# Optimization experiments

Measured on AMD Instinct MI355X. Metric: run time of the kernel, lower is better.

The kernel has to match this reference:

```python
import jax, jax.numpy as jnp
import numpy as np

B, T, D, H, L, V, CTX = 4, 2048, 256, 8, 12, 256, 2048
HD = D // H


def _ln(x, w, b, eps=1e-5):
    m = x.mean(-1, keepdims=True)
    v = ((x - m) ** 2).mean(-1, keepdims=True)
    return (x - m) * jax.lax.rsqrt(v + eps) * w + b


def setup_inputs() -> dict:
    key = jax.random.key(0)
    ks = jax.random.split(key, 16)
    s = 0.02
    inp = {
        "x": jax.random.randint(ks[0], (B, T), 0, V, dtype=jnp.int32),
        "tok_embed": jax.random.normal(ks[1], (V, D), jnp.float32) * s,
        "pos_embed": jax.random.normal(ks[2], (CTX, D), jnp.float32) * s,
        # stacked per-layer params (leading axis = layer)
        "ln1_w": jnp.ones((L, D), jnp.float32),
        "ln1_b": jnp.zeros((L, D), jnp.float32),
        "qkv_w": jax.random.normal(ks[3], (L, D, 3 * D), jnp.float32) * s,
        "qkv_b": jnp.zeros((L, 3 * D), jnp.float32),
        "out_w": jax.random.normal(ks[4], (L, D, D), jnp.float32) * s,
        "out_b": jnp.zeros((L, D), jnp.float32),
        "ln2_w": jnp.ones((L, D), jnp.float32),
        "ln2_b": jnp.zeros((L, D), jnp.float32),
        "fc1_w": jax.random.normal(ks[5], (L, D, 4 * D), jnp.float32) * s,
        "fc1_b": jnp.zeros((L, 4 * D), jnp.float32),
        "fc2_w": jax.random.normal(ks[6], (L, 4 * D, D), jnp.float32) * s,
        "fc2_b": jnp.zeros((L, D), jnp.float32),
        "lnf_w": jnp.ones((D,), jnp.float32),
        "lnf_b": jnp.zeros((D,), jnp.float32),
        "head_w": jax.random.normal(ks[7], (D, V), jnp.float32) * s,
        "head_b": jnp.zeros((V,), jnp.float32),
    }
    return inp


def _forward(x, tok_embed, pos_embed, ln1_w, ln1_b, qkv_w, qkv_b, out_w, out_b,
             ln2_w, ln2_b, fc1_w, fc1_b, fc2_w, fc2_b, lnf_w, lnf_b, head_w, head_b):
    Tcur = x.shape[1]
    h = tok_embed[x] + pos_embed[:Tcur][None, :, :]  # (B,T,D)
    causal = jnp.triu(jnp.ones((Tcur, Tcur), bool), k=1)  # True above diagonal
    scale = jnp.sqrt(jnp.asarray(HD, h.dtype))

    def step(h, p):
        (l1w, l1b, qw, qb, ow, ob, l2w, l2b, f1w, f1b, f2w, f2b) = p
        # attention
        z = _ln(h, l1w, l1b)
        qkv = z @ qw + qb  # (B,T,3D)
        qkv = qkv.reshape(h.shape[0], Tcur, 3, H, HD)
        q, k, v = qkv[:, :, 0], qkv[:, :, 1], qkv[:, :, 2]  # (B,T,H,HD)
        attn = jnp.einsum('bqhd,bkhd->bhqk', q, k) / scale
        attn = jnp.where(causal, -jnp.inf, attn)
        attn = jax.nn.softmax(attn, axis=-1)
        o = jnp.einsum('bhqk,bkhd->bqhd', attn, v).reshape(h.shape[0], Tcur, D)
        h = h + o @ ow + ob
        # MLP (torch nn.GELU default = exact erf gelu)
        z = _ln(h, l2w, l2b)
        z = jax.nn.gelu(z @ f1w + f1b, approximate=False)
        h = h + z @ f2w + f2b
        return h, None

    params = (ln1_w, ln1_b, qkv_w, qkv_b, out_w, out_b,
              ln2_w, ln2_b, fc1_w, fc1_b, fc2_w, fc2_b)
    h, _ = jax.lax.scan(step, h, params)
    h = _ln(h, lnf_w, lnf_b)
    return h @ head_w + head_b  # (B,T,V)


def reference(x, tok_embed, pos_embed, ln1_w, ln1_b, qkv_w, qkv_b, out_w, out_b,
              ln2_w, ln2_b, fc1_w, fc1_b, fc2_w, fc2_b, lnf_w, lnf_b, head_w, head_b):
    return _forward(x, tok_embed, pos_embed, ln1_w, ln1_b, qkv_w, qkv_b, out_w, out_b,
                    ln2_w, ln2_b, fc1_w, fc1_b, fc2_w, fc2_b, lnf_w, lnf_b, head_w, head_b)
```

## Files before the change

kernel.cpp:

```cpp
#include <hip/hip_runtime.h>
#include <cstdint>

#define TT 2048
#define DD 256
#define HH 8
#define LL 12

typedef __attribute__((ext_vector_type(8))) short s16x8;
typedef __attribute__((ext_vector_type(4))) float f32x4;

__device__ __forceinline__ unsigned short f2bf(float f) {
  union { float f; unsigned u; } v; v.f = f;
  return (unsigned short)((v.u + 0x7FFFu + ((v.u >> 16) & 1u)) >> 16);
}

__device__ __forceinline__ unsigned cvtpk(float lo, float hi) {
  unsigned r;
  asm("v_cvt_pk_bf16_f32 %0, %1, %2" : "=v"(r) : "v"(lo), "v"(hi));
  return r;
}

__device__ __forceinline__ float geluf(float x) {
  return 0.5f * x * (1.0f + erff(x * 0.70710678118654752f));
}

__device__ __forceinline__ float fexp2(float x) {
  float r;
  asm("v_exp_f32 %0, %1" : "=v"(r) : "v"(x));
  return r;
}

__device__ __forceinline__ void gload16(const void* g, void* l) {
  __builtin_amdgcn_global_load_lds((const __attribute__((address_space(1))) unsigned int*)g,
                                   (__attribute__((address_space(3))) unsigned int*)l, 16, 0, 0);
}

__global__ __launch_bounds__(256) void k_embed_ln(const int* __restrict__ x,
                                                  const float* __restrict__ tok,
                                                  const float* __restrict__ pos,
                                                  const float* __restrict__ wgt,
                                                  const float* __restrict__ bia,
                                                  float* __restrict__ h,
                                                  unsigned short* __restrict__ z) {
  int row = blockIdx.x * 4 + (threadIdx.x >> 6);
  int lane = threadIdx.x & 63;
  int t = x[row];
  f32x4 tv = ((const f32x4*)(tok + (size_t)t * DD))[lane];
  f32x4 pv = ((const f32x4*)(pos + (size_t)(row & (TT - 1)) * DD))[lane];
  f32x4 v = tv + pv;
  ((f32x4*)(h + (size_t)row * DD))[lane] = v;
  float s = v[0] + v[1] + v[2] + v[3];
#pragma unroll
  for (int m = 32; m; m >>= 1) s += __shfl_xor(s, m);
  float mean = s * (1.0f / DD);
  f32x4 d = v - mean;
  float s2 = d[0] * d[0] + d[1] * d[1] + d[2] * d[2] + d[3] * d[3];
#pragma unroll
  for (int m = 32; m; m >>= 1) s2 += __shfl_xor(s2, m);
  float inv = rsqrtf(s2 * (1.0f / DD) + 1e-5f);
  f32x4 wv = ((const f32x4*)wgt)[lane];
  f32x4 bv = ((const f32x4*)bia)[lane];
  float o0 = d[0] * inv * wv[0] + bv[0], o1 = d[1] * inv * wv[1] + bv[1];
  float o2 = d[2] * inv * wv[2] + bv[2], o3 = d[3] * inv * wv[3] + bv[3];
  unsigned long long u64 = (unsigned long long)cvtpk(o0, o1) |
                           ((unsigned long long)cvtpk(o2, o3) << 32);
  *(unsigned long long*)(z + (size_t)row * DD + lane * 4) = u64;
}

__global__ __launch_bounds__(256) void k_cast_all(const float* __restrict__ qw, const float* __restrict__ ow,
                                                  const float* __restrict__ f1, const float* __restrict__ f2,
                                                  const float* __restrict__ hw,
                                                  unsigned short* __restrict__ dst) {
  __shared__ float Tt[32][33];
  const int l = blockIdx.y;
  const int t = blockIdx.x;
  const float* src;
  unsigned short* d;
  int K, N, tk, tn;
  if (l == 12) {
    if (t >= 64) return;
    src = hw; d = dst + (size_t)12 * 786432;
    K = 256; N = 256; tk = t >> 3; tn = t & 7;
  } else if (t < 192) {
    src = qw + (size_t)l * 196608; d = dst + (size_t)l * 786432;
    K = 256; N = 768; tk = t / 24; tn = t % 24;
  } else if (t < 256) {
    int t2 = t - 192;
    src = ow + (size_t)l * 65536; d = dst + (size_t)l * 786432 + 196608;
    K = 256; N = 256; tk = t2 >> 3; tn = t2 & 7;
  } else if (t < 512) {
    int t3 = t - 256;
    src = f1 + (size_t)l * 262144; d = dst + (size_t)l * 786432 + 262144;
    K = 256; N = 1024; tk = t3 >> 5; tn = t3 & 31;
  } else {
    int t4 = t - 512;
    src = f2 + (size_t)l * 262144; d = dst + (size_t)l * 786432 + 524288;
    K = 1024; N = 256; tk = t4 >> 3; tn = t4 & 7;
  }
  const int tx = threadIdx.x & 31, ty = threadIdx.x >> 5;
#pragma unroll
  for (int r = 0; r < 4; ++r) {
    int row = ty + r * 8;
    Tt[row][tx] = src[(size_t)(tk * 32 + row) * N + tn * 32 + tx];
  }
  __syncthreads();
#pragma unroll
  for (int r = 0; r < 4; ++r) {
    int row = ty + r * 8;
    d[(size_t)(tn * 32 + row) * K + tk * 32 + tx] = f2bf(Tt[tx][row]);
  }
}

__global__ __launch_bounds__(256) void k_cast_tr4(const float* __restrict__ qw, const float* __restrict__ ow,
                                                  const float* __restrict__ f1, const float* __restrict__ f2,
                                                  unsigned short* __restrict__ dq, unsigned short* __restrict__ dO,
                                                  unsigned short* __restrict__ d1, unsigned short* __restrict__ d2) {
  int t0 = blockIdx.x * 256 + threadIdx.x;
  int stride = gridDim.x * 256;
  for (int i = t0; i < 196608; i += stride) dq[i] = f2bf(qw[(i & 255) * 768 + (i >> 8)]);
  for (int i = t0; i < 65536; i += stride) dO[i] = f2bf(ow[(i & 255) * 256 + (i >> 8)]);
  for (int i = t0; i < 262144; i += stride) d1[i] = f2bf(f1[(i & 255) * 1024 + (i >> 8)]);
  for (int i = t0; i < 262144; i += stride) d2[i] = f2bf(f2[(i & 1023) * 256 + (i >> 10)]);
}

__global__ __launch_bounds__(256) void k_cast_tr256(const float* __restrict__ src, unsigned short* __restrict__ dst) {
  int i = blockIdx.x * 256 + threadIdx.x;
  dst[i] = f2bf(src[(i & 255) * 256 + (i >> 8)]);
}

template <int MODE, int MI>
__global__ __launch_bounds__(256, 3) void k_gemm(const unsigned short* __restrict__ A,
                                                 const unsigned short* __restrict__ BT,
                                                 const float* __restrict__ bias,
                                                 void* out, const float* resid,
                                                 int M, int N, int K) {
  __shared__ __align__(16) unsigned short As[2][MI * 32 * 64];
  __shared__ __align__(16) unsigned short Bs[2][128 * 64];
  const int tid = threadIdx.x;
  const int lane = tid & 63, wv = tid >> 6;
  const int wr = wv >> 1, wc = wv & 1;
  const int l15 = lane & 15, g = lane >> 4;
  const int BM = MI * 32;
  const int tm = blockIdx.y, tn = blockIdx.x;
  f32x4 acc[MI][4] = {};
  const int nk = K >> 6;
  const unsigned short* Ag0 = A + (size_t)tm * BM * K;
  const unsigned short* Bg0 = BT + (size_t)tn * 128 * K;

#pragma unroll
  for (int it = 0; it < MI; ++it) {
    int c = it * 256 + tid;
    gload16(Ag0 + (size_t)(c >> 3) * K + (c & 7) * 8, As[0] + c * 8);
  }
#pragma unroll
  for (int it = 0; it < 4; ++it) {
    int c = it * 256 + tid;
    gload16(Bg0 + (size_t)(c >> 3) * K + (c & 7) * 8, Bs[0] + c * 8);
  }
  __syncthreads();

  int buf = 0;
  for (int kt = 0; kt < nk; ++kt) {
    const bool have_next = (kt + 1 < nk);
    if (have_next) {
#pragma unroll
      for (int it = 0; it < MI; ++it) {
        int c = it * 256 + tid;
        gload16(Ag0 + (size_t)(c >> 3) * K + (kt + 1) * 64 + (c & 7) * 8, As[buf ^ 1] + c * 8);
      }
#pragma unroll
      for (int it = 0; it < 4; ++it) {
        int c = it * 256 + tid;
        gload16(Bg0 + (size_t)(c >> 3) * K + (kt + 1) * 64 + (c & 7) * 8, Bs[buf ^ 1] + c * 8);
      }
    }
#pragma unroll
    for (int ks = 0; ks < 2; ++ks) {
      s16x8 af[MI], bf[4];
#pragma unroll
      for (int mi = 0; mi < MI; ++mi)
        af[mi] = *(const s16x8*)(As[buf] + (wr * MI * 16 + mi * 16 + l15) * 64 + ks * 32 + g * 8);
#pragma unroll
      for (int ni = 0; ni < 4; ++ni)
        bf[ni] = *(const s16x8*)(Bs[buf] + (wc * 64 + ni * 16 + l15) * 64 + ks * 32 + g * 8);
#pragma unroll
      for (int mi = 0; mi < MI; ++mi)
#pragma unroll
        for (int ni = 0; ni < 4; ++ni)
          acc[mi][ni] = __builtin_amdgcn_mfma_f32_16x16x32_bf16(af[mi], bf[ni], acc[mi][ni], 0, 0, 0);
    }
    if (have_next) {
      __syncthreads();
      buf ^= 1;
    }
  }
#pragma unroll
  for (int ni = 0; ni < 4; ++ni) {
    int col = tn * 128 + wc * 64 + ni * 16 + l15;
    float bv = bias[col];
#pragma unroll
    for (int mi = 0; mi < MI; ++mi) {
      int row0 = tm * BM + wr * MI * 16 + mi * 16 + g * 4;
#pragma unroll
      for (int r = 0; r < 4; ++r) {
        size_t idx = (size_t)(row0 + r) * N + col;
        float vvv = acc[mi][ni][r] + bv;
        if (MODE == 0) ((unsigned short*)out)[idx] = f2bf(vvv);
        else if (MODE == 1) ((unsigned short*)out)[idx] = f2bf(geluf(vvv));
        else ((float*)out)[idx] = vvv;
      }
    }
  }
}

template <int NK>
__global__ __launch_bounds__(512, 2) void k_gemm_ln(const unsigned short* __restrict__ A,
                                                    const unsigned short* __restrict__ BT,
                                                    const float* __restrict__ bias,
                                                    float* __restrict__ h,
                                                    const float* __restrict__ lnw,
                                                    const float* __restrict__ lnb,
                                                    unsigned short* __restrict__ z) {
  __shared__ __align__(16) unsigned short As[2][32 * 64];
  __shared__ __align__(16) unsigned short Bs[2][256 * 64];
  const int tid = threadIdx.x;
  const int lane = tid & 63, wc = tid >> 6;
  const int l15 = lane & 15, g = lane >> 4;
  const int tm = blockIdx.x;
  const int K = NK * 64;
  const int row0 = tm * 32;
  f32x4 acc[2][2] = {};
  const unsigned short* Ag0 = A + (size_t)tm * 32 * K;

  float rv[2][2][4];
#pragma unroll
  for (int mi = 0; mi < 2; ++mi)
#pragma unroll
    for (int ni = 0; ni < 2; ++ni) {
      int col = wc * 32 + ni * 16 + l15;
#pragma unroll
      for (int r = 0; r < 4; ++r)
        rv[mi][ni][r] = h[(size_t)(row0 + mi * 16 + g * 4 + r) * DD + col];
    }

  if (tid < 256) gload16(Ag0 + (size_t)(tid >> 3) * K + (tid & 7) * 8, As[0] + tid * 8);
#pragma unroll
  for (int it = 0; it < 4; ++it) {
    int c = it * 512 + tid;
    gload16(BT + (size_t)(c >> 3) * K + (c & 7) * 8, Bs[0] + c * 8);
  }
  __syncthreads();

  int buf = 0;
  for (int kt = 0; kt < NK; ++kt) {
    const bool have_next = (kt + 1 < NK);
    if (have_next) {
      if (tid < 256)
        gload16(Ag0 + (size_t)(tid >> 3) * K + (kt + 1) * 64 + (tid & 7) * 8, As[buf ^ 1] + tid * 8);
#pragma unroll
      for (int it = 0; it < 4; ++it) {
        int c = it * 512 + tid;
        gload16(BT + (size_t)(c >> 3) * K + (kt + 1) * 64 + (c & 7) * 8, Bs[buf ^ 1] + c * 8);
      }
    }
#pragma unroll
    for (int ks = 0; ks < 2; ++ks) {
      s16x8 af[2], bf[2];
#pragma unroll
      for (int mi = 0; mi < 2; ++mi)
        af[mi] = *(const s16x8*)(As[buf] + (mi * 16 + l15) * 64 + ks * 32 + g * 8);
#pragma unroll
      for (int ni = 0; ni < 2; ++ni)
        bf[ni] = *(const s16x8*)(Bs[buf] + (wc * 32 + ni * 16 + l15) * 64 + ks * 32 + g * 8);
#pragma unroll
      for (int mi = 0; mi < 2; ++mi)
#pragma unroll
        for (int ni = 0; ni < 2; ++ni)
          acc[mi][ni] = __builtin_amdgcn_mfma_f32_16x16x32_bf16(af[mi], bf[ni], acc[mi][ni], 0, 0, 0);
    }
    if (have_next) {
      __syncthreads();
      buf ^= 1;
    }
  }
  float hv[2][2][4];
  float psum[2][4] = {}, psq[2][4] = {};
#pragma unroll
  for (int mi = 0; mi < 2; ++mi)
#pragma unroll
    for (int ni = 0; ni < 2; ++ni) {
      int col = wc * 32 + ni * 16 + l15;
      float bv = bias[col];
#pragma unroll
      for (int r = 0; r < 4; ++r) {
        int row = row0 + mi * 16 + g * 4 + r;
        float v = acc[mi][ni][r] + bv + rv[mi][ni][r];
        hv[mi][ni][r] = v;
        h[(size_t)row * DD + col] = v;
        psum[mi][r] += v;
        psq[mi][r] += v * v;
      }
    }
#pragma unroll
  for (int m = 1; m < 16; m <<= 1)
#pragma unroll
    for (int mi = 0; mi < 2; ++mi)
#pragma unroll
      for (int r = 0; r < 4; ++r) {
        psum[mi][r] += __shfl_xor(psum[mi][r], m);
        psq[mi][r] += __shfl_xor(psq[mi][r], m);
      }
  __syncthreads();
  float* red = (float*)&As[0][0];
  if (l15 == 0) {
#pragma unroll
    for (int mi = 0; mi < 2; ++mi)
#pragma unroll
      for (int r = 0; r < 4; ++r) {
        int rw = mi * 16 + g * 4 + r;
        red[wc * 32 + rw] = psum[mi][r];
        red[256 + wc * 32 + rw] = psq[mi][r];
      }
  }
  __syncthreads();
  float mean[2][4], inv[2][4];
#pragma unroll
  for (int mi = 0; mi < 2; ++mi)
#pragma unroll
    for (int r = 0; r < 4; ++r) {
      int rw = mi * 16 + g * 4 + r;
      float s = 0.f, q = 0.f;
#pragma unroll
      for (int wv = 0; wv < 8; ++wv) {
        s += red[wv * 32 + rw];
        q += red[256 + wv * 32 + rw];
      }
      float mn = s * (1.0f / DD);
      mean[mi][r] = mn;
      inv[mi][r] = rsqrtf(q * (1.0f / DD) - mn * mn + 1e-5f);
    }
#pragma unroll
  for (int ni = 0; ni < 2; ++ni) {
    int col = wc * 32 + ni * 16 + l15;
    float wvv = lnw[col], bvv = lnb[col];
#pragma unroll
    for (int mi = 0; mi < 2; ++mi)
#pragma unroll
      for (int r = 0; r < 4; ++r) {
        int row = row0 + mi * 16 + g * 4 + r;
        z[(size_t)row * DD + col] = f2bf((hv[mi][ni][r] - mean[mi][r]) * inv[mi][r] * wvv + bvv);
      }
  }
}

__global__ __launch_bounds__(512, 4) void k_attn(const unsigned short* __restrict__ qkv,
                                                 unsigned short* __restrict__ o) {
  __shared__ __align__(16) unsigned short Ks[2][128 * 40];
  __shared__ __align__(16) unsigned short Vs[2][2 * 32 * 72];
  const int tid = threadIdx.x, lane = tid & 63, wvi = tid >> 6;
  const int w = wvi >> 1, kh = wvi & 1;
  const int l15 = lane & 15, g = lane >> 4;
  const int p = blockIdx.x;
  const int b = blockIdx.y >> 3, hh = blockIdx.y & 7;
  const size_t base = (size_t)b * TT * 768 + hh * 32;
  const float scl2 = 0.25503492f;
  const int qt0 = p, qt1 = 31 - p;
  const int nt0 = (qt0 >> 1) + 1;
  const int krow = (wvi & 3) * 32 + (lane >> 1);
  const int khK = lane & 1;
  const int iv = wvi & 3;
  const int khv = iv >> 1, dh = iv & 1;

  s16x8 qf0 = *(const s16x8*)(qkv + base + (size_t)(qt0 * 64 + w * 16 + l15) * 768 + g * 8);
  s16x8 qf1 = *(const s16x8*)(qkv + base + (size_t)(qt1 * 64 + w * 16 + l15) * 768 + g * 8);

  if (wvi < 4) {
    const unsigned short* kp = qkv + base + (size_t)krow * 768 + 256 + khK * 16;
    s16x8 k0 = *(const s16x8*)kp;
    s16x8 k1 = *(const s16x8*)(kp + 8);
    *(s16x8*)(Ks[0] + krow * 40 + khK * 16) = k0;
    *(s16x8*)(Ks[0] + krow * 40 + khK * 16 + 8) = k1;
  } else {
    const unsigned short* vp = qkv + base + (size_t)(khv * 64 + lane) * 768 + 512 + dh * 16;
    s16x8 v0 = *(const s16x8*)vp;
    s16x8 v1 = *(const s16x8*)(vp + 8);
    unsigned short* vb = Vs[0] + khv * 2304;
#pragma unroll
    for (int e = 0; e < 8; ++e) {
      int d0 = dh * 16 + e, d1 = dh * 16 + 8 + e;
      vb[d0 * 72 + (lane ^ (((d0 >> 3) & 3) << 4))] = (unsigned short)v0[e];
      vb[d1 * 72 + (lane ^ (((d1 >> 3) & 3) << 4))] = (unsigned short)v1[e];
    }
  }
  __syncthreads();

  f32x4 accO[2] = {};
  float mM = -3.0e38f, ls = 0.f;

  for (int t = 0; t < 17; ++t) {
    const int buf = t & 1;
    const bool ph = (t >= nt0);
    const int qt = ph ? qt1 : qt0;
    const int j = ph ? t - nt0 : t;
    const bool have_next = (t + 1 < 17);
    unsigned short* ps = (wvi < 4) ? (Ks[buf ^ 1] + wvi * 1280)
                                   : (Vs[buf ^ 1] + (wvi - 4) * 1152);
    s16x8 k0n, k1n, v0n, v1n;
    if (have_next) {
      const int jn = (t + 1 >= nt0) ? t + 1 - nt0 : t + 1;
      if (wvi < 4) {
        const unsigned short* kp = qkv + base + (size_t)(jn * 128 + krow) * 768 + 256 + khK * 16;
        k0n = *(const s16x8*)kp;
        k1n = *(const s16x8*)(kp + 8);
      } else {
        const unsigned short* vp = qkv + base + (size_t)(jn * 128 + khv * 64 + lane) * 768 + 512 + dh * 16;
        v0n = *(const s16x8*)vp;
        v1n = *(const s16x8*)(vp + 8);
      }
    }
    const int rel = qt * 64 + w * 16 - j * 128;
    int cbg = (rel + 15) >> 4; if (cbg > 7) cbg = 7;
    const int cbm = (cbg - kh * 4 > 3) ? 3 : cbg - kh * 4;
    if (cbm >= 0) {
      const bool fullw = (rel >= kh * 64 + 63);
      f32x4 st[4];
#pragma unroll
      for (int c = 0; c < 4; ++c)
        if (c <= cbm) {
          s16x8 kf = *(const s16x8*)(Ks[buf] + (kh * 64 + c * 16 + l15) * 40 + g * 8);
          f32x4 zz = {};
          st[c] = __builtin_amdgcn_mfma_f32_16x16x32_bf16(kf, ph ? qf1 : qf0, zz, 0, 0, 0);
        }
      float rmax = -3.0e38f;
#pragma unroll
      for (int c = 0; c < 4; ++c)
        if (c <= cbm) {
          if (!fullw) {
#pragma unroll
            for (int r = 0; r < 4; ++r)
              if ((kh * 64 + c * 16 + g * 4 + r) > rel + l15) st[c][r] = -3.0e38f;
          }
#pragma unroll
          for (int r = 0; r < 4; ++r) rmax = fmaxf(rmax, st[c][r]);
        }
      rmax = fmaxf(rmax, __shfl_xor(rmax, 16));
      rmax = fmaxf(rmax, __shfl_xor(rmax, 32));
      const float rs = rmax * scl2;
      float al = 1.0f;
      if (!__all(rs <= mM + 11.5f)) {
        float nm = fmaxf(mM, rs);
        al = fexp2(mM - nm);
        mM = nm;
#pragma unroll
        for (int r = 0; r < 4; ++r) {
          float aw = __shfl(al, g * 4 + r);
          accO[0][r] *= aw;
          accO[1][r] *= aw;
        }
      }
      float rsum = 0.f;
#pragma unroll
      for (int c = 0; c < 4; ++c)
        if (c <= cbm) {
          float e0 = fexp2(fmaf(st[c][0], scl2, -mM));
          float e1 = fexp2(fmaf(st[c][1], scl2, -mM));
          float e2 = fexp2(fmaf(st[c][2], scl2, -mM));
          float e3 = fexp2(fmaf(st[c][3], scl2, -mM));
          rsum += (e0 + e1) + (e2 + e3);
          unsigned long long u = (unsigned long long)cvtpk(e0, e1) |
                                 ((unsigned long long)cvtpk(e2, e3) << 32);
          *(unsigned long long*)(ps + l15 * 72 + c * 16 + g * 4) = u;
        }
      if (cbm < 3 && !(cbm & 1))
        *(unsigned long long*)(ps + l15 * 72 + (cbm + 1) * 16 + g * 4) = 0ULL;
      rsum += __shfl_xor(rsum, 16);
      rsum += __shfl_xor(rsum, 32);
      ls = ls * al + rsum;
      asm volatile("s_waitcnt lgkmcnt(0)" ::: "memory");
      __builtin_amdgcn_sched_barrier(0);
      const int kcm = cbm >> 1;
#pragma unroll
      for (int kc = 0; kc < 2; ++kc)
        if (kc <= kcm) {
          s16x8 pa = *(const s16x8*)(ps + l15 * 72 + kc * 32 + g * 8);
          s16x8 bv0, bv1;
#pragma unroll
          for (int hb = 0; hb < 2; ++hb) {
            const int d = hb * 16 + l15;
            const int kx = (kc * 32 + g * 8) ^ (((d >> 3) & 3) << 4);
            if (hb == 0) bv0 = *(const s16x8*)(Vs[buf] + kh * 2304 + d * 72 + kx);
            else bv1 = *(const s16x8*)(Vs[buf] + kh * 2304 + d * 72 + kx);
          }
          accO[0] = __builtin_amdgcn_mfma_f32_16x16x32_bf16(pa, bv0, accO[0], 0, 0, 0);
          accO[1] = __builtin_amdgcn_mfma_f32_16x16x32_bf16(pa, bv1, accO[1], 0, 0, 0);
        }
    }
    if (have_next) {
      if (wvi < 4) {
        *(s16x8*)(Ks[buf ^ 1] + krow * 40 + khK * 16) = k0n;
        *(s16x8*)(Ks[buf ^ 1] + krow * 40 + khK * 16 + 8) = k1n;
      } else {
        unsigned short* vb = Vs[buf ^ 1] + khv * 2304;
#pragma unroll
        for (int e = 0; e < 8; ++e) {
          int d0 = dh * 16 + e, d1 = dh * 16 + 8 + e;
          vb[d0 * 72 + (lane ^ (((d0 >> 3) & 3) << 4))] = (unsigned short)v0n[e];
          vb[d1 * 72 + (lane ^ (((d1 >> 3) & 3) << 4))] = (unsigned short)v1n[e];
        }
      }
      __syncthreads();
    }
    if (t == nt0 - 1) {
      float* sc = (float*)((wvi < 4) ? (Ks[buf] + wvi * 1280) : (Vs[buf] + (wvi - 4) * 1152));
#pragma unroll
      for (int hb = 0; hb < 2; ++hb)
#pragma unroll
        for (int r = 0; r < 4; ++r) sc[(g * 4 + r) * 32 + hb * 16 + l15] = accO[hb][r];
      if (g == 0) { sc[512 + l15] = mM; sc[528 + l15] = ls; }
      __syncthreads();
      if (kh == 0) {
        const int pw = wvi + 1;
        float* pb = (float*)((pw < 4) ? (Ks[buf] + pw * 1280) : (Vs[buf] + (pw - 4) * 1152));
#pragma unroll
        for (int r = 0; r < 4; ++r) {
          int q = g * 4 + r;
          float mA = __shfl(mM, q), lA = __shfl(ls, q);
          float mB = pb[512 + q], lB = pb[528 + q];
          float M = fmaxf(mA, mB);
          float eA = fexp2(mA - M), eB = fexp2(mB - M);
          float inv = 1.0f / (eA * lA + eB * lB);
          int row = qt0 * 64 + w * 16 + q;
#pragma unroll
          for (int hb = 0; hb < 2; ++hb) {
            float ob = pb[q * 32 + hb * 16 + l15];
            float val = (eA * accO[hb][r] + eB * ob) * inv;
            o[(size_t)(b * TT + row) * DD + hh * 32 + hb * 16 + l15] = f2bf(val);
          }
        }
      }
      __syncthreads();
      accO[0] = f32x4{};
      accO[1] = f32x4{};
      mM = -3.0e38f;
      ls = 0.f;
    }
  }
  {
    __syncthreads();
    float* sc = (float*)((wvi < 4) ? (Ks[0] + wvi * 1280) : (Vs[0] + (wvi - 4) * 1152));
#pragma unroll
    for (int hb = 0; hb < 2; ++hb)
#pragma unroll
      for (int r = 0; r < 4; ++r) sc[(g * 4 + r) * 32 + hb * 16 + l15] = accO[hb][r];
    if (g == 0) { sc[512 + l15] = mM; sc[528 + l15] = ls; }
    __syncthreads();
    if (kh == 0) {
      const int pw = wvi + 1;
      float* pb = (float*)((pw < 4) ? (Ks[0] + pw * 1280) : (Vs[0] + (pw - 4) * 1152));
#pragma unroll
      for (int r = 0; r < 4; ++r) {
        int q = g * 4 + r;
        float mA = __shfl(mM, q), lA = __shfl(ls, q);
        float mB = pb[512 + q], lB = pb[528 + q];
        float M = fmaxf(mA, mB);
        float eA = fexp2(mA - M), eB = fexp2(mB - M);
        float inv = 1.0f / (eA * lA + eB * lB);
        int row = qt1 * 64 + w * 16 + q;
#pragma unroll
        for (int hb = 0; hb < 2; ++hb) {
          float ob = pb[q * 32 + hb * 16 + l15];
          float val = (eA * accO[hb][r] + eB * ob) * inv;
          o[(size_t)(b * TT + row) * DD + hh * 32 + hb * 16 + l15] = f2bf(val);
        }
      }
    }
  }
}

extern "C" void kernel_launch(void* const* d_in, const int* in_sizes, int n_in,
                              void* d_out, int out_size, void* d_ws, size_t ws_size,
                              hipStream_t stream) {
  const int* x = (const int*)d_in[0];
  const float* tok = (const float*)d_in[1];
  const float* pos = (const float*)d_in[2];
  const float* ln1w = (const float*)d_in[3];
  const float* ln1b = (const float*)d_in[4];
  const float* qkvw = (const float*)d_in[5];
  const float* qkvb = (const float*)d_in[6];
  const float* outw = (const float*)d_in[7];
  const float* outb = (const float*)d_in[8];
  const float* ln2w = (const float*)d_in[9];
  const float* ln2b = (const float*)d_in[10];
  const float* f1w = (const float*)d_in[11];
  const float* f1b = (const float*)d_in[12];
  const float* f2w = (const float*)d_in[13];
  const float* f2b = (const float*)d_in[14];
  const float* lnfw = (const float*)d_in[15];
  const float* lnfb = (const float*)d_in[16];
  const float* hw = (const float*)d_in[17];
  const float* hb = (const float*)d_in[18];

  char* ws = (char*)d_ws;
  float* h = (float*)(ws + 0);
  unsigned short* z = (unsigned short*)(ws + 8388608);
  unsigned short* qkvB = (unsigned short*)(ws + 12582912);
  unsigned short* ob = (unsigned short*)(ws + 25165824);
  unsigned short* a1 = (unsigned short*)(ws + 29360128);
  unsigned short* wAll = (unsigned short*)(ws + 46137344);
  const bool bigws = ws_size >= 65142784ULL;
  unsigned short* wh = (unsigned short*)(ws + (bigws ? 65011712 : 47710208));

  if (bigws)
    k_cast_all<<<dim3(768, 13), dim3(256), 0, stream>>>(qkvw, outw, f1w, f2w, hw, wAll);
  else
    k_cast_tr256<<<dim3(256), dim3(256), 0, stream>>>(hw, wh);
  k_embed_ln<<<dim3(2048), dim3(256), 0, stream>>>(x, tok, pos, ln1w, ln1b, h, z);

  for (int l = 0; l < LL; ++l) {
    unsigned short* wq = wAll + (size_t)(bigws ? l : 0) * 786432;
    unsigned short* wo = wq + 196608;
    unsigned short* w1 = wo + 65536;
    unsigned short* w2 = w1 + 262144;
    if (!bigws)
      k_cast_tr4<<<dim3(1024), dim3(256), 0, stream>>>(
          qkvw + (size_t)l * 196608, outw + (size_t)l * 65536,
          f1w + (size_t)l * 262144, f2w + (size_t)l * 262144, wq, wo, w1, w2);
    k_gemm<0, 2><<<dim3(6, 128), dim3(256), 0, stream>>>(z, wq, qkvb + l * 768, qkvB, nullptr, 8192, 768, 256);
    k_attn<<<dim3(16, 32), dim3(512), 0, stream>>>(qkvB, ob);
    k_gemm_ln<4><<<dim3(256), dim3(512), 0, stream>>>(ob, wo, outb + l * 256, h,
                                                      ln2w + l * 256, ln2b + l * 256, z);
    k_gemm<1, 2><<<dim3(8, 128), dim3(256), 0, stream>>>(z, w1, f1b + l * 1024, a1, nullptr, 8192, 1024, 256);
    const float* nw = (l == LL - 1) ? lnfw : ln1w + (l + 1) * 256;
    const float* nb = (l == LL - 1) ? lnfb : ln1b + (l + 1) * 256;
    k_gemm_ln<16><<<dim3(256), dim3(512), 0, stream>>>(a1, w2, f2b + l * 256, h, nw, nb, z);
  }

  k_gemm<3, 2><<<dim3(2, 128), dim3(256), 0, stream>>>(z, wh, hb, d_out, nullptr, 8192, 256, 256);
}
```

Measured before the change: 1.292 ms.

## Split attention KV loop across two blocks with separate combine kernel

```diff
diff --git a/kernel.cpp b/kernel.cpp
--- a/kernel.cpp
+++ b/kernel.cpp
@@ -354,18 +354,21 @@
 }
 
 __global__ __launch_bounds__(512, 4) void k_attn(const unsigned short* __restrict__ qkv,
-                                                 unsigned short* __restrict__ o) {
+                                                 float* __restrict__ part,
+                                                 float* __restrict__ ml) {
   __shared__ __align__(16) unsigned short Ks[2][128 * 40];
   __shared__ __align__(16) unsigned short Vs[2][2 * 32 * 72];
   const int tid = threadIdx.x, lane = tid & 63, wvi = tid >> 6;
   const int w = wvi >> 1, kh = wvi & 1;
   const int l15 = lane & 15, g = lane >> 4;
-  const int p = blockIdx.x;
+  const int p = blockIdx.x >> 1, rep = blockIdx.x & 1;
   const int b = blockIdx.y >> 3, hh = blockIdx.y & 7;
   const size_t base = (size_t)b * TT * 768 + hh * 32;
+  const size_t bh0 = (size_t)(b * 8 + hh) * 2048;
   const float scl2 = 0.25503492f;
   const int qt0 = p, qt1 = 31 - p;
   const int nt0 = (qt0 >> 1) + 1;
+  const int nit = (18 - rep) >> 1;
   const int krow = (wvi & 3) * 32 + (lane >> 1);
   const int khK = lane & 1;
   const int iv = wvi & 3;
@@ -374,14 +377,15 @@
   s16x8 qf0 = *(const s16x8*)(qkv + base + (size_t)(qt0 * 64 + w * 16 + l15) * 768 + g * 8);
   s16x8 qf1 = *(const s16x8*)(qkv + base + (size_t)(qt1 * 64 + w * 16 + l15) * 768 + g * 8);
 
+  const int j0 = (rep >= nt0) ? rep - nt0 : rep;
   if (wvi < 4) {
-    const unsigned short* kp = qkv + base + (size_t)krow * 768 + 256 + khK * 16;
+    const unsigned short* kp = qkv + base + (size_t)(j0 * 128 + krow) * 768 + 256 + khK * 16;
     s16x8 k0 = *(const s16x8*)kp;
     s16x8 k1 = *(const s16x8*)(kp + 8);
     *(s16x8*)(Ks[0] + krow * 40 + khK * 16) = k0;
     *(s16x8*)(Ks[0] + krow * 40 + khK * 16 + 8) = k1;
   } else {
-    const unsigned short* vp = qkv + base + (size_t)(khv * 64 + lane) * 768 + 512 + dh * 16;
+    const unsigned short* vp = qkv + base + (size_t)(j0 * 128 + khv * 64 + lane) * 768 + 512 + dh * 16;
     s16x8 v0 = *(const s16x8*)vp;
     s16x8 v1 = *(const s16x8*)(vp + 8);
     unsigned short* vb = Vs[0] + khv * 2304;
@@ -394,20 +398,35 @@
   }
   __syncthreads();
 
+  if (rep == 1 && nt0 == 1 && kh == 0) {
+#pragma unroll
+    for (int r = 0; r < 4; ++r) {
+      size_t bq = bh0 + qt0 * 64 + w * 16 + g * 4 + r;
+      part[(65536ull + bq) * 32 + l15] = 0.f;
+      part[(65536ull + bq) * 32 + 16 + l15] = 0.f;
+      if (l15 == 0) {
+        ml[(65536ull + bq) * 2] = -3.0e38f;
+        ml[(65536ull + bq) * 2 + 1] = 0.f;
+      }
+    }
+  }
+
   f32x4 accO[2] = {};
   float mM = -3.0e38f, ls = 0.f;
 
-  for (int t = 0; t < 17; ++t) {
-    const int buf = t & 1;
+  for (int tt = 0; tt < nit; ++tt) {
+    const int t = rep + 2 * tt;
+    const int buf = tt & 1;
     const bool ph = (t >= nt0);
     const int qt = ph ? qt1 : qt0;
     const int j = ph ? t - nt0 : t;
-    const bool have_next = (t + 1 < 17);
+    const bool have_next = (tt + 1 < nit);
     unsigned short* ps = (wvi < 4) ? (Ks[buf ^ 1] + wvi * 1280)
                                    : (Vs[buf ^ 1] + (wvi - 4) * 1152);
     s16x8 k0n, k1n, v0n, v1n;
     if (have_next) {
-      const int jn = (t + 1 >= nt0) ? t + 1 - nt0 : t + 1;
+      const int tn = t + 2;
+      const int jn = (tn >= nt0) ? tn - nt0 : tn;
       if (wvi < 4) {
         const unsigned short* kp = qkv + base + (size_t)(jn * 128 + krow) * 768 + 256 + khK * 16;
         k0n = *(const s16x8*)kp;
@@ -510,7 +529,7 @@
       }
       __syncthreads();
     }
-    if (t == nt0 - 1) {
+    if (t < nt0 && t + 2 >= nt0) {
       float* sc = (float*)((wvi < 4) ? (Ks[buf] + wvi * 1280) : (Vs[buf] + (wvi - 4) * 1152));
 #pragma unroll
       for (int hb = 0; hb < 2; ++hb)
@@ -528,13 +547,15 @@
           float mB = pb[512 + q], lB = pb[528 + q];
           float M = fmaxf(mA, mB);
           float eA = fexp2(mA - M), eB = fexp2(mB - M);
-          float inv = 1.0f / (eA * lA + eB * lB);
-          int row = qt0 * 64 + w * 16 + q;
+          size_t bq = bh0 + qt0 * 64 + w * 16 + q;
 #pragma unroll
           for (int hb = 0; hb < 2; ++hb) {
-            float ob = pb[q * 32 + hb * 16 + l15];
-            float val = (eA * accO[hb][r] + eB * ob) * inv;
-            o[(size_t)(b * TT + row) * DD + hh * 32 + hb * 16 + l15] = f2bf(val);
+            float ob_ = pb[q * 32 + hb * 16 + l15];
+            part[((size_t)rep * 65536 + bq) * 32 + hb * 16 + l15] = eA * accO[hb][r] + eB * ob_;
+          }
+          if (l15 == 0) {
+            ml[((size_t)rep * 65536 + bq) * 2] = M;
+            ml[((size_t)rep * 65536 + bq) * 2 + 1] = eA * lA + eB * lB;
           }
         }
       }
@@ -546,8 +567,9 @@
     }
   }
   {
+    const int fb = (nit - 1) & 1;
     __syncthreads();
-    float* sc = (float*)((wvi < 4) ? (Ks[0] + wvi * 1280) : (Vs[0] + (wvi - 4) * 1152));
+    float* sc = (float*)((wvi < 4) ? (Ks[fb] + wvi * 1280) : (Vs[fb] + (wvi - 4) * 1152));
 #pragma unroll
     for (int hb = 0; hb < 2; ++hb)
 #pragma unroll
@@ -556,7 +578,7 @@
     __syncthreads();
     if (kh == 0) {
       const int pw = wvi + 1;
-      float* pb = (float*)((pw < 4) ? (Ks[0] + pw * 1280) : (Vs[0] + (pw - 4) * 1152));
+      float* pb = (float*)((pw < 4) ? (Ks[fb] + pw * 1280) : (Vs[fb] + (pw - 4) * 1152));
 #pragma unroll
       for (int r = 0; r < 4; ++r) {
         int q = g * 4 + r;
@@ -564,17 +586,39 @@
         float mB = pb[512 + q], lB = pb[528 + q];
         float M = fmaxf(mA, mB);
         float eA = fexp2(mA - M), eB = fexp2(mB - M);
-        float inv = 1.0f / (eA * lA + eB * lB);
-        int row = qt1 * 64 + w * 16 + q;
+        size_t bq = bh0 + qt1 * 64 + w * 16 + q;
 #pragma unroll
         for (int hb = 0; hb < 2; ++hb) {
-          float ob = pb[q * 32 + hb * 16 + l15];
-          float val = (eA * accO[hb][r] + eB * ob) * inv;
-          o[(size_t)(b * TT + row) * DD + hh * 32 + hb * 16 + l15] = f2bf(val);
-        }
-      }
-    }
-  }
+          float ob_ = pb[q * 32 + hb * 16 + l15];
+          part[((size_t)rep * 65536 + bq) * 32 + hb * 16 + l15] = eA * accO[hb][r] + eB * ob_;
+        }
+        if (l15 == 0) {
+          ml[((size_t)rep * 65536 + bq) * 2] = M;
+          ml[((size_t)rep * 65536 + bq) * 2 + 1] = eA * lA + eB * lB;
+        }
+      }
+    }
+  }
+}
+
+__global__ __launch_bounds__(256) void k_acomb(const float* __restrict__ part,
+                                               const float* __restrict__ ml,
+                                               unsigned short* __restrict__ ob) {
+  int gid = blockIdx.x * 256 + threadIdx.x;
+  int row = gid >> 3, dq = gid & 7;
+  float m0 = ml[(size_t)row * 2], l0 = ml[(size_t)row * 2 + 1];
+  float m1 = ml[(65536ull + row) * 2], l1 = ml[(65536ull + row) * 2 + 1];
+  float M = fmaxf(m0, m1);
+  float e0 = fexp2(m0 - M), e1 = fexp2(m1 - M);
+  float inv = 1.0f / (e0 * l0 + e1 * l1);
+  f32x4 O0 = ((const f32x4*)(part + (size_t)row * 32))[dq];
+  f32x4 O1 = ((const f32x4*)(part + (65536ull + row) * 32))[dq];
+  int b = row >> 14, hh = (row >> 11) & 7, q = row & 2047;
+  float v0 = (e0 * O0[0] + e1 * O1[0]) * inv, v1 = (e0 * O0[1] + e1 * O1[1]) * inv;
+  float v2 = (e0 * O0[2] + e1 * O1[2]) * inv, v3 = (e0 * O0[3] + e1 * O1[3]) * inv;
+  unsigned long long u = (unsigned long long)cvtpk(v0, v1) |
+                         ((unsigned long long)cvtpk(v2, v3) << 32);
+  *(unsigned long long*)(ob + ((size_t)(b * 2048 + q) * 256 + hh * 32 + dq * 4)) = u;
 }
 
 extern "C" void kernel_launch(void* const* d_in, const int* in_sizes, int n_in,
@@ -609,6 +653,8 @@
   unsigned short* wAll = (unsigned short*)(ws + 46137344);
   const bool bigws = ws_size >= 65142784ULL;
   unsigned short* wh = (unsigned short*)(ws + (bigws ? 65011712 : 47710208));
+  float* part = (float*)a1;
+  float* ml = (float*)z;
 
   if (bigws)
     k_cast_all<<<dim3(768, 13), dim3(256), 0, stream>>>(qkvw, outw, f1w, f2w, hw, wAll);
@@ -626,7 +672,8 @@
           qkvw + (size_t)l * 196608, outw + (size_t)l * 65536,
           f1w + (size_t)l * 262144, f2w + (size_t)l * 262144, wq, wo, w1, w2);
     k_gemm<0, 2><<<dim3(6, 128), dim3(256), 0, stream>>>(z, wq, qkvb + l * 768, qkvB, nullptr, 8192, 768, 256);
-    k_attn<<<dim3(16, 32), dim3(512), 0, stream>>>(qkvB, ob);
+    k_attn<<<dim3(32, 32), dim3(512), 0, stream>>>(qkvB, part, ml);
+    k_acomb<<<dim3(2048), dim3(256), 0, stream>>>(part, ml, ob);
     k_gemm_ln<4><<<dim3(256), dim3(512), 0, stream>>>(ob, wo, outb + l * 256, h,
                                                       ln2w + l * 256, ln2b + l * 256, z);
     k_gemm<1, 2><<<dim3(8, 128), dim3(256), 0, stream>>>(z, w1, f1b + l * 1024, a1, nullptr, 8192, 1024, 256);
```

After: 1.473 ms. 1.14x slower.
